# Kernel optimization log

Measured on AMD Instinct MI355X. Metric: run time of the kernel, lower is better.

The kernel has to match this reference:

```python
import jax, jax.numpy as jnp
import numpy as np

B, T, C, N = 4, 1024, 960, 64
H = C // N
R_W, R_A, R_V, R_G = 64, 64, 32, 128
LN_EPS = 0.00064


def setup_inputs() -> dict:
    key = jax.random.key(0)
    ks = jax.random.split(key, 28)
    s = 0.5 / np.sqrt(C)
    u = lambda k, sh, sc: jax.random.uniform(k, sh, jnp.float32, -sc, sc)
    n = lambda k, sh, sc: jax.random.normal(k, sh, jnp.float32) * sc
    return {
        "x": jax.random.normal(ks[0], (B, T, C), jnp.float32),
        "v_first": jax.random.normal(ks[1], (B, T, C), jnp.float32),
        "x_r": jax.random.uniform(ks[2], (1, 1, C), jnp.float32),
        "x_w": jax.random.uniform(ks[3], (1, 1, C), jnp.float32),
        "x_k": jax.random.uniform(ks[4], (1, 1, C), jnp.float32),
        "x_v": jax.random.uniform(ks[5], (1, 1, C), jnp.float32),
        "x_a": jax.random.uniform(ks[6], (1, 1, C), jnp.float32),
        "x_g": jax.random.uniform(ks[7], (1, 1, C), jnp.float32),
        "w0": n(ks[8], (1, 1, C), 0.5) - 2.0,
        "w1": n(ks[9], (C, R_W), 0.02),
        "w2": n(ks[10], (R_W, C), 0.02),
        "a0": n(ks[11], (1, 1, C), 0.3),
        "a1": n(ks[12], (C, R_A), 0.02),
        "a2": n(ks[13], (R_A, C), 0.02),
        "v0": n(ks[14], (1, 1, C), 0.3) + 0.73,
        "v1": n(ks[15], (C, R_V), 0.02),
        "v2": n(ks[16], (R_V, C), 0.02),
        "g1": n(ks[17], (C, R_G), 0.02),
        "g2": n(ks[18], (R_G, C), 0.02),
        "k_k": n(ks[19], (1, 1, C), 0.1) + 0.71,
        "k_a": n(ks[20], (1, 1, C), 0.1) + 1.02,
        "r_k": n(ks[21], (H, N), 0.1) - 0.04,
        "Wr": u(ks[22], (C, C), s),
        "Wk": u(ks[23], (C, C), 0.1 * s),
        "Wv": u(ks[24], (C, C), s),
        "Wo": u(ks[25], (C, C), s),
        "ln_g": jnp.ones((C,), jnp.float32),
        "ln_b": jnp.zeros((C,), jnp.float32),
    }


def reference(x, v_first, x_r, x_w, x_k, x_v, x_a, x_g, w0, w1, w2,
              a0, a1, a2, v0, v1, v2, g1, g2, k_k, k_a, r_k,
              Wr, Wk, Wv, Wo, ln_g, ln_b):
    Bx, Tx, Cx = x.shape
    # token shift: xx[t] = x[t-1] - x[t], with x[-1] = 0
    xx = jnp.concatenate([jnp.zeros_like(x[:, :1]), x[:, :-1]], axis=1) - x
    xr = x + xx * x_r; xw = x + xx * x_w; xk = x + xx * x_k
    xv = x + xx * x_v; xa = x + xx * x_a; xg = x + xx * x_g
    r = xr @ Wr
    w_raw = w0 + jnp.tanh(xw @ w1) @ w2       # log-space decay
    k = xk @ Wk
    v = xv @ Wv
    # layer_id > 0: residual mix with layer-0 value
    v = v + (v_first - v) * jax.nn.sigmoid(v0 + (xv @ v1) @ v2)
    a = jax.nn.sigmoid(a0 + (xa @ a1) @ a2)   # in-context learning rate
    g = jax.nn.sigmoid(xg @ g1) @ g2          # gate
    kk = (k * k_k).reshape(Bx, Tx, H, N)
    kk = kk / jnp.maximum(jnp.linalg.norm(kk, axis=-1, keepdims=True), 1e-12)
    k = k * (1.0 + (a - 1.0) * k_a)
    f32 = jnp.float32
    rh = r.reshape(Bx, Tx, H, N).astype(f32)
    kh = k.reshape(Bx, Tx, H, N).astype(f32)
    vh = v.reshape(Bx, Tx, H, N).astype(f32)
    wh = jnp.exp(-jax.nn.softplus(-w_raw.reshape(Bx, Tx, H, N).astype(f32)) - 0.5)
    ah = (-kk).astype(f32)                              # removal key
    bh = (kk * a.reshape(Bx, Tx, H, N)).astype(f32)     # replacement key

    def step(state, inp):
        r_t, w_t, k_t, v_t, a_t, b_t = inp  # each (B,H,N); state (B,H,N,N)
        sa = jnp.einsum('bhij,bhj->bhi', state, a_t)
        state = (state * w_t[:, :, None, :]
                 + sa[..., None] * b_t[:, :, None, :]
                 + v_t[..., None] * k_t[:, :, None, :])
        out_t = jnp.einsum('bhij,bhj->bhi', state, r_t)
        return state, out_t

    tm = lambda u: jnp.transpose(u, (1, 0, 2, 3))  # time-major
    state0 = jnp.zeros((Bx, H, N, N), f32)
    _, wkv = jax.lax.scan(step, state0, (tm(rh), tm(wh), tm(kh), tm(vh), tm(ah), tm(bh)))
    wkv = jnp.transpose(wkv, (1, 0, 2, 3))  # (B,T,H,N)
    # GroupNorm with H groups == per-head layernorm over N
    mu = wkv.mean(-1, keepdims=True)
    var = wkv.var(-1, keepdims=True)
    xn = (wkv - mu) / jnp.sqrt(var + LN_EPS)
    xn = xn * ln_g.reshape(H, N) + ln_b.reshape(H, N)
    bonus = (rh * kh * r_k).sum(-1, keepdims=True) * vh  # r*k*v bonus term
    xo = (xn + bonus).astype(x.dtype).reshape(Bx, Tx, Cx)
    return (xo * g) @ Wo


if __name__ == "__main__":
    out = reference(**setup_inputs())
    print(out.shape, out.dtype)
```

## Files before the change

kernel.cpp:

```cpp
#include <hip/hip_runtime.h>
#include <hip/hip_bf16.h>
#include <math.h>

#define Tn 1024
#define Cn 960
#define Hn 15
#define Nn 64
#define Mn 4096

typedef short bf16x8 __attribute__((ext_vector_type(8)));
typedef float f32x4 __attribute__((ext_vector_type(4)));

#define MCc ((size_t)Mn * Cn)

__device__ __forceinline__ float sigmf(float x) { return 1.0f / (1.0f + __expf(-x)); }

__device__ __forceinline__ ushort f2bf(float x) {
    unsigned u = __float_as_uint(x);
    unsigned r = (u + 0x7FFFu + ((u >> 16) & 1u)) >> 16;
    return (ushort)r;
}
__device__ __forceinline__ float bf2f(ushort h) { return __uint_as_float(((unsigned)h) << 16); }

__device__ __forceinline__ float rowsum16(float x) {
    x += __int_as_float(__builtin_amdgcn_update_dpp(0, __float_as_int(x), 0x121, 0xF, 0xF, true));
    x += __int_as_float(__builtin_amdgcn_update_dpp(0, __float_as_int(x), 0x122, 0xF, 0xF, true));
    x += __int_as_float(__builtin_amdgcn_update_dpp(0, __float_as_int(x), 0x124, 0xF, 0xF, true));
    x += __int_as_float(__builtin_amdgcn_update_dpp(0, __float_as_int(x), 0x128, 0xF, 0xF, true));
    return x;
}

__global__ __launch_bounds__(256) void mix6_kernel(
    const float* __restrict__ x,
    const float* __restrict__ mr, const float* __restrict__ mw, const float* __restrict__ mk,
    const float* __restrict__ mv, const float* __restrict__ ma, const float* __restrict__ mg,
    ushort* __restrict__ r_sp, ushort* __restrict__ w_sp, ushort* __restrict__ k_sp,
    ushort* __restrict__ v_sp, ushort* __restrict__ a_sp, ushort* __restrict__ g_sp)
{
    int idx = blockIdx.x * 256 + threadIdx.x;
    int e = idx * 4;
    if (e >= Mn * Cn) return;
    int m = e / Cn;
    int c = e - m * Cn;
    int t = m & (Tn - 1);
    float4 xv = *(const float4*)(x + e);
    float4 xp = make_float4(0.f, 0.f, 0.f, 0.f);
    if (t > 0) xp = *(const float4*)(x + e - Cn);
    float4 dx = make_float4(xp.x - xv.x, xp.y - xv.y, xp.z - xv.z, xp.w - xv.w);
#define MIXSPLIT(MIXP, P)                                                     \
    {                                                                         \
        float4 mm = *(const float4*)(MIXP + c);                               \
        float4 O = make_float4(xv.x + dx.x * mm.x, xv.y + dx.y * mm.y,        \
                               xv.z + dx.z * mm.z, xv.w + dx.w * mm.w);       \
        ushort h0 = f2bf(O.x), h1 = f2bf(O.y), h2 = f2bf(O.z), h3 = f2bf(O.w);\
        ushort l0 = f2bf(O.x - bf2f(h0)), l1 = f2bf(O.y - bf2f(h1));          \
        ushort l2 = f2bf(O.z - bf2f(h2)), l3 = f2bf(O.w - bf2f(h3));          \
        *(ushort4*)(P + e) = make_ushort4(h0, h1, h2, h3);                    \
        *(ushort4*)(P + MCc + e) = make_ushort4(l0, l1, l2, l3);              \
    }
    MIXSPLIT(mr, r_sp)
    MIXSPLIT(mw, w_sp)
    MIXSPLIT(mk, k_sp)
    MIXSPLIT(mv, v_sp)
    MIXSPLIT(ma, a_sp)
    MIXSPLIT(mg, g_sp)
#undef MIXSPLIT
}

__global__ __launch_bounds__(256) void convWT_kernel(
    const float* __restrict__ W, ushort* __restrict__ Thi, ushort* __restrict__ Tlo)
{
    __shared__ float tile[32][33];
    int k0 = blockIdx.x * 32, n0 = blockIdx.y * 32;
    int tx = threadIdx.x & 31, ty = threadIdx.x >> 5;
#pragma unroll
    for (int i = 0; i < 4; ++i)
        tile[ty + 8 * i][tx] = W[(size_t)(k0 + ty + 8 * i) * 960 + n0 + tx];
    __syncthreads();
#pragma unroll
    for (int i = 0; i < 4; ++i) {
        float x = tile[tx][ty + 8 * i];
        ushort h = f2bf(x);
        ushort l = f2bf(x - bf2f(h));
        size_t o = (size_t)(n0 + ty + 8 * i) * 960 + k0 + tx;
        Thi[o] = h;
        Tlo[o] = l;
    }
}

__global__ __launch_bounds__(256) void convWT3_kernel(
    const float* __restrict__ Wr, const float* __restrict__ Wk,
    const float* __restrict__ Wv,
    ushort* __restrict__ S0, ushort* __restrict__ S1, ushort* __restrict__ S2)
{
    __shared__ float tile[32][33];
    int z = blockIdx.z;
    const float* W = (z == 0) ? Wr : (z == 1) ? Wk : Wv;
    ushort* Thi = (z == 0) ? S0 : (z == 1) ? S1 : S2;
    ushort* Tlo = Thi + (size_t)960 * 960;
    int k0 = blockIdx.x * 32, n0 = blockIdx.y * 32;
    int tx = threadIdx.x & 31, ty = threadIdx.x >> 5;
#pragma unroll
    for (int i = 0; i < 4; ++i)
        tile[ty + 8 * i][tx] = W[(size_t)(k0 + ty + 8 * i) * 960 + n0 + tx];
    __syncthreads();
#pragma unroll
    for (int i = 0; i < 4; ++i) {
        float x = tile[tx][ty + 8 * i];
        ushort h = f2bf(x);
        ushort l = f2bf(x - bf2f(h));
        size_t o = (size_t)(n0 + ty + 8 * i) * 960 + k0 + tx;
        Thi[o] = h;
        Tlo[o] = l;
    }
}

__global__ __launch_bounds__(256) void wprep_kernel(
    const float* __restrict__ w1, const float* __restrict__ a1,
    const float* __restrict__ v1, const float* __restrict__ g1,
    const float* __restrict__ w2, const float* __restrict__ a2,
    const float* __restrict__ v2, const float* __restrict__ g2,
    ushort* __restrict__ arena)
{
    __shared__ float tile[32][33];
    int z = blockIdx.z;
    const float* src;
    int K, N;
    size_t off;
    switch (z) {
        case 0: src = w1; K = 960; N = 64;  off = 0;      break;
        case 1: src = a1; K = 960; N = 64;  off = 122880; break;
        case 2: src = v1; K = 960; N = 32;  off = 245760; break;
        case 3: src = g1; K = 960; N = 128; off = 307200; break;
        case 4: src = w2; K = 64;  N = 960; off = 552960; break;
        case 5: src = a2; K = 64;  N = 960; off = 675840; break;
        case 6: src = v2; K = 32;  N = 960; off = 798720; break;
        default: src = g2; K = 128; N = 960; off = 860160; break;
    }
    int k0 = blockIdx.x * 32, n0 = blockIdx.y * 32;
    if (k0 >= K || n0 >= N) return;
    int tx = threadIdx.x & 31, ty = threadIdx.x >> 5;
#pragma unroll
    for (int i = 0; i < 4; ++i)
        tile[ty + 8 * i][tx] = src[(size_t)(k0 + ty + 8 * i) * N + n0 + tx];
    __syncthreads();
    ushort* Thi = arena + off;
    ushort* Tlo = arena + off + (size_t)K * N;
#pragma unroll
    for (int i = 0; i < 4; ++i) {
        float x = tile[tx][ty + 8 * i];
        ushort h = f2bf(x);
        ushort l = f2bf(x - bf2f(h));
        size_t o = (size_t)(n0 + ty + 8 * i) * K + k0 + tx;
        Thi[o] = h;
        Tlo[o] = l;
    }
}

__global__ __launch_bounds__(256) void convN_kernel(
    const float* __restrict__ X, ushort* __restrict__ hi, ushort* __restrict__ lo, int n4)
{
    int idx = blockIdx.x * 256 + threadIdx.x;
    if (idx >= n4) return;
    int e = idx * 4;
    float4 x = *(const float4*)(X + e);
    ushort h0 = f2bf(x.x), h1 = f2bf(x.y), h2 = f2bf(x.z), h3 = f2bf(x.w);
    ushort l0 = f2bf(x.x - bf2f(h0)), l1 = f2bf(x.y - bf2f(h1));
    ushort l2 = f2bf(x.z - bf2f(h2)), l3 = f2bf(x.w - bf2f(h3));
    *(ushort4*)(hi + e) = make_ushort4(h0, h1, h2, h3);
    *(ushort4*)(lo + e) = make_ushort4(l0, l1, l2, l3);
}

__device__ __forceinline__ void gemm_core(
    const ushort* __restrict__ Ahi, const ushort* __restrict__ Alo,
    const ushort* __restrict__ Bhi, const ushort* __restrict__ Blo,
    float* __restrict__ C, int ldc, int bm, int bn)
{
    __shared__ __align__(16) ushort sA[2][2][128][40];
    __shared__ __align__(16) ushort sB[2][2][64][40];
    const int K = 960;
    int t = threadIdx.x;
    int w = t >> 6, l = t & 63;
    int lr = l & 15, lk = l >> 4;

    int ar = t >> 1, aseg = t & 1;
    int br = t & 63, bhalf = (t >> 6) & 1, bseg = t >> 7;
    const ushort* gAh = Ahi + (size_t)(bm + ar) * K + aseg * 16;
    const ushort* gAl = Alo + (size_t)(bm + ar) * K + aseg * 16;
    const ushort* gB = (bhalf ? Blo : Bhi) + (size_t)(bn + br) * K + bseg * 16;

    f32x4 acc[2][4];
#pragma unroll
    for (int i = 0; i < 2; ++i)
#pragma unroll
        for (int j = 0; j < 4; ++j)
#pragma unroll
            for (int e = 0; e < 4; ++e) acc[i][j][e] = 0.f;

    float4 h0P, h1P, l0P, l1P, b0P, b1P;
    float4 h0Q, h1Q, l0Q, l1Q, b0Q, b1Q;
#define LOADP(KOFF)                                                           \
    {                                                                         \
        h0P = *(const float4*)(gAh + (KOFF));                                 \
        h1P = *(const float4*)(gAh + (KOFF) + 8);                             \
        l0P = *(const float4*)(gAl + (KOFF));                                 \
        l1P = *(const float4*)(gAl + (KOFF) + 8);                             \
        b0P = *(const float4*)(gB + (KOFF));                                  \
        b1P = *(const float4*)(gB + (KOFF) + 8);                              \
    }
#define LOADQ(KOFF)                                                           \
    {                                                                         \
        h0Q = *(const float4*)(gAh + (KOFF));                                 \
        h1Q = *(const float4*)(gAh + (KOFF) + 8);                             \
        l0Q = *(const float4*)(gAl + (KOFF));                                 \
        l1Q = *(const float4*)(gAl + (KOFF) + 8);                             \
        b0Q = *(const float4*)(gB + (KOFF));                                  \
        b1Q = *(const float4*)(gB + (KOFF) + 8);                              \
    }
#define WRITEP(BUF)                                                           \
    {                                                                         \
        *(float4*)&sA[BUF][0][ar][aseg * 16] = h0P;                           \
        *(float4*)&sA[BUF][0][ar][aseg * 16 + 8] = h1P;                       \
        *(float4*)&sA[BUF][1][ar][aseg * 16] = l0P;                           \
        *(float4*)&sA[BUF][1][ar][aseg * 16 + 8] = l1P;                       \
        *(float4*)&sB[BUF][bhalf][br][bseg * 16] = b0P;                       \
        *(float4*)&sB[BUF][bhalf][br][bseg * 16 + 8] = b1P;                   \
    }
#define WRITEQ(BUF)                                                           \
    {                                                                         \
        *(float4*)&sA[BUF][0][ar][aseg * 16] = h0Q;                           \
        *(float4*)&sA[BUF][0][ar][aseg * 16 + 8] = h1Q;                       \
        *(float4*)&sA[BUF][1][ar][aseg * 16] = l0Q;                           \
        *(float4*)&sA[BUF][1][ar][aseg * 16 + 8] = l1Q;                       \
        *(float4*)&sB[BUF][bhalf][br][bseg * 16] = b0Q;                       \
        *(float4*)&sB[BUF][bhalf][br][bseg * 16 + 8] = b1Q;                   \
    }
#define COMPUTEK(BUF)                                                         \
    {                                                                         \
        bf16x8 ah[2], al[2], bh[4], bl[4];                                    \
        _Pragma("unroll")                                                     \
        for (int i = 0; i < 2; ++i) {                                         \
            ah[i] = *(const bf16x8*)&sA[BUF][0][32 * w + 16 * i + lr][lk * 8];\
            al[i] = *(const bf16x8*)&sA[BUF][1][32 * w + 16 * i + lr][lk * 8];\
        }                                                                     \
        _Pragma("unroll")                                                     \
        for (int j = 0; j < 4; ++j) {                                         \
            bh[j] = *(const bf16x8*)&sB[BUF][0][16 * j + lr][lk * 8];         \
            bl[j] = *(const bf16x8*)&sB[BUF][1][16 * j + lr][lk * 8];         \
        }                                                                     \
        _Pragma("unroll")                                                     \
        for (int i = 0; i < 2; ++i)                                           \
            _Pragma("unroll")                                                 \
            for (int j = 0; j < 4; ++j) {                                     \
                acc[i][j] = __builtin_amdgcn_mfma_f32_16x16x32_bf16(          \
                    ah[i], bh[j], acc[i][j], 0, 0, 0);                        \
                acc[i][j] = __builtin_amdgcn_mfma_f32_16x16x32_bf16(          \
                    ah[i], bl[j], acc[i][j], 0, 0, 0);                        \
                acc[i][j] = __builtin_amdgcn_mfma_f32_16x16x32_bf16(          \
                    al[i], bh[j], acc[i][j], 0, 0, 0);                        \
            }                                                                 \
    }

    LOADP(0)
    WRITEP(0)
    LOADQ(32)
    asm volatile("s_waitcnt lgkmcnt(0)" ::: "memory");
    __builtin_amdgcn_s_barrier();

    int cur = 0;
    for (int ks = 0; ks < 30; ks += 2) {
        int k2 = (ks + 2 < 30 ? ks + 2 : 29) * 32;
        LOADP(k2)
        COMPUTEK(cur)
        WRITEQ(cur ^ 1)
        asm volatile("s_waitcnt lgkmcnt(0)" ::: "memory");
        __builtin_amdgcn_s_barrier();
        cur ^= 1;
        int k3 = (ks + 3 < 30 ? ks + 3 : 29) * 32;
        LOADQ(k3)
        COMPUTEK(cur)
        WRITEP(cur ^ 1)
        asm volatile("s_waitcnt lgkmcnt(0)" ::: "memory");
        __builtin_amdgcn_s_barrier();
        cur ^= 1;
    }

#pragma unroll
    for (int i = 0; i < 2; ++i)
#pragma unroll
        for (int j = 0; j < 4; ++j)
#pragma unroll
            for (int jr = 0; jr < 4; ++jr) {
                int row = bm + 32 * w + 16 * i + lk * 4 + jr;
                int col = bn + 16 * j + lr;
                C[(size_t)row * ldc + col] = acc[i][j][jr];
            }
#undef COMPUTEK
#undef WRITEP
#undef WRITEQ
#undef LOADP
#undef LOADQ
}

__global__ __launch_bounds__(256) void gemm3_kernel(
    const ushort* __restrict__ XR, const ushort* __restrict__ XK,
    const ushort* __restrict__ XV,
    const ushort* __restrict__ WrS, const ushort* __restrict__ WkS,
    const ushort* __restrict__ WvS,
    float* __restrict__ oR, float* __restrict__ oK, float* __restrict__ oV)
{
    int z = blockIdx.z;
    const ushort* A = (z == 0) ? XR : (z == 1) ? XK : XV;
    const ushort* W = (z == 0) ? WrS : (z == 1) ? WkS : WvS;
    float* C = (z == 0) ? oR : (z == 1) ? oK : oV;
    gemm_core(A, A + MCc, W, W + (size_t)960 * 960, C, Cn,
              blockIdx.x * 128, blockIdx.y * 64);
}

__global__ __launch_bounds__(256) void gemm1_kernel(
    const ushort* __restrict__ Ahi, const ushort* __restrict__ Alo,
    const ushort* __restrict__ Bhi, const ushort* __restrict__ Blo,
    float* __restrict__ C, int ldc)
{
    gemm_core(Ahi, Alo, Bhi, Blo, C, ldc, blockIdx.x * 128, blockIdx.y * 64);
}

__device__ __forceinline__ void lora_core(
    const ushort* __restrict__ Ahi, const ushort* __restrict__ Alo, int lda,
    const ushort* __restrict__ Bhi, const ushort* __restrict__ Blo,
    float* __restrict__ C, int ldc, int Nvalid, int K, int act, int bn)
{
    __shared__ __align__(16) ushort sA[2][2][128][40];
    __shared__ __align__(16) ushort sB[2][2][64][40];
    int bm = blockIdx.x * 128;
    int t = threadIdx.x;
    int w = t >> 6, l = t & 63;
    int lr = l & 15, lk = l >> 4;

    int ar = t >> 2, aseg = t & 3;
    int brr = t >> 2;
    int bhl = brr >> 6, brow = brr & 63, bseg = t & 3;
    const ushort* gAh = Ahi + (size_t)(bm + ar) * lda + aseg * 8;
    const ushort* gAl = Alo + (size_t)(bm + ar) * lda + aseg * 8;
    const ushort* gB = (bhl ? Blo : Bhi) + (size_t)(bn + brow) * K + bseg * 8;

    f32x4 acc[4];
#pragma unroll
    for (int j = 0; j < 4; ++j)
#pragma unroll
        for (int e = 0; e < 4; ++e) acc[j][e] = 0.f;

    float4 rhP, rlP, rbP, rhQ, rlQ, rbQ;
#define LLOADP(KOFF)                                                          \
    {                                                                         \
        rhP = *(const float4*)(gAh + (KOFF));                                 \
        rlP = *(const float4*)(gAl + (KOFF));                                 \
        rbP = *(const float4*)(gB + (KOFF));                                  \
    }
#define LLOADQ(KOFF)                                                          \
    {                                                                         \
        rhQ = *(const float4*)(gAh + (KOFF));                                 \
        rlQ = *(const float4*)(gAl + (KOFF));                                 \
        rbQ = *(const float4*)(gB + (KOFF));                                  \
    }
#define LWRITEP(BUF)                                                          \
    {                                                                         \
        *(float4*)&sA[BUF][0][ar][aseg * 8] = rhP;                            \
        *(float4*)&sA[BUF][1][ar][aseg * 8] = rlP;                            \
        *(float4*)&sB[BUF][bhl][brow][bseg * 8] = rbP;                        \
    }
#define LWRITEQ(BUF)                                                          \
    {                                                                         \
        *(float4*)&sA[BUF][0][ar][aseg * 8] = rhQ;                            \
        *(float4*)&sA[BUF][1][ar][aseg * 8] = rlQ;                            \
        *(float4*)&sB[BUF][bhl][brow][bseg * 8] = rbQ;                        \
    }
#define LCOMPUTE(BUF)                                                         \
    {                                                                         \
        bf16x8 ah, al, bh[4], bl[4];                                          \
        ah = *(const bf16x8*)&sA[BUF][0][16 * w + lr][lk * 8];                \
        al = *(const bf16x8*)&sA[BUF][1][16 * w + lr][lk * 8];                \
        _Pragma("unroll")                                                     \
        for (int j = 0; j < 4; ++j) {                                         \
            bh[j] = *(const bf16x8*)&sB[BUF][0][16 * j + lr][lk * 8];         \
            bl[j] = *(const bf16x8*)&sB[BUF][1][16 * j + lr][lk * 8];         \
        }                                                                     \
        _Pragma("unroll")                                                     \
        for (int j = 0; j < 4; ++j) {                                         \
            acc[j] = __builtin_amdgcn_mfma_f32_16x16x32_bf16(ah, bh[j], acc[j], 0, 0, 0); \
            acc[j] = __builtin_amdgcn_mfma_f32_16x16x32_bf16(ah, bl[j], acc[j], 0, 0, 0); \
            acc[j] = __builtin_amdgcn_mfma_f32_16x16x32_bf16(al, bh[j], acc[j], 0, 0, 0); \
        }                                                                     \
    }

    int nk = K >> 5;
    LLOADP(0)
    LWRITEP(0)
    if (nk > 1) LLOADQ(32)
    asm volatile("s_waitcnt lgkmcnt(0)" ::: "memory");
    __builtin_amdgcn_s_barrier();

    int cur = 0;
    for (int ks = 0; ks < nk; ++ks) {
        int k2 = (ks + 2 < nk ? ks + 2 : nk - 1) * 32;
        if (!(ks & 1)) { LLOADP(k2) } else { LLOADQ(k2) }
        LCOMPUTE(cur)
        if (ks + 1 < nk) {
            if (!(ks & 1)) { LWRITEQ(cur ^ 1) } else { LWRITEP(cur ^ 1) }
            asm volatile("s_waitcnt lgkmcnt(0)" ::: "memory");
            __builtin_amdgcn_s_barrier();
        }
        cur ^= 1;
    }

#pragma unroll
    for (int j = 0; j < 4; ++j)
#pragma unroll
        for (int jr = 0; jr < 4; ++jr) {
            int row = bm + 16 * w + lk * 4 + jr;
            int col = bn + 16 * j + lr;
            if (col < Nvalid) {
                float v = acc[j][jr];
                if (act == 1) v = tanhf(v);
                else if (act == 2) v = sigmf(v);
                C[(size_t)row * ldc + col] = v;
            }
        }
#undef LCOMPUTE
#undef LWRITEP
#undef LWRITEQ
#undef LLOADP
#undef LLOADQ
}

__global__ __launch_bounds__(512) void lora_down_kernel(
    const ushort* __restrict__ xw_sp, const ushort* __restrict__ xa_sp,
    const ushort* __restrict__ xv_sp, const ushort* __restrict__ xg_sp,
    const ushort* __restrict__ arena, float* __restrict__ hid)
{
    int z = blockIdx.z;
    int bn = blockIdx.y * 64;
    const ushort* A;
    size_t off;
    int N, act, coff;
    switch (z) {
        case 0: A = xw_sp; off = 0;      N = 64;  act = 1; coff = 0;   break;
        case 1: A = xa_sp; off = 122880; N = 64;  act = 0; coff = 64;  break;
        case 2: A = xv_sp; off = 245760; N = 32;  act = 0; coff = 128; break;
        default: A = xg_sp; off = 307200; N = 128; act = 2; coff = 160; break;
    }
    if (bn >= N) return;
    lora_core(A, A + MCc, Cn, arena + off, arena + off + (size_t)960 * N,
              hid + coff, 288, N, 960, act, bn);
}

__global__ __launch_bounds__(512) void lora_up_kernel(
    const ushort* __restrict__ hidHi, const ushort* __restrict__ hidLo,
    const ushort* __restrict__ arena,
    float* __restrict__ oW, float* __restrict__ oA,
    float* __restrict__ oV, float* __restrict__ oG)
{
    int z = blockIdx.z;
    int bn = blockIdx.y * 64;
    size_t off;
    int K, aoff;
    float* C;
    switch (z) {
        case 0: off = 552960; K = 64;  aoff = 0;   C = oW; break;
        case 1: off = 675840; K = 64;  aoff = 64;  C = oA; break;
        case 2: off = 798720; K = 32;  aoff = 128; C = oV; break;
        default: off = 860160; K = 128; aoff = 160; C = oG; break;
    }
    lora_core(hidHi + aoff, hidLo + aoff, 288, arena + off,
              arena + off + (size_t)K * 960, C, Cn, Cn, K, 0, bn);
}

__global__ __launch_bounds__(256, 2) void scan_kernel(
    const float* __restrict__ rP, const float* __restrict__ wrawP,
    const float* __restrict__ apreP, const float* __restrict__ vsigP,
    const float* __restrict__ krawP, const float* __restrict__ vrawP,
    const float* __restrict__ vfirstP, const float* __restrict__ gP,
    const float* __restrict__ w0, const float* __restrict__ a0,
    const float* __restrict__ v0c, const float* __restrict__ kkc,
    const float* __restrict__ kac, const float* __restrict__ r_k,
    const float* __restrict__ ln_g, const float* __restrict__ ln_b,
    ushort* __restrict__ xsp)
{
    __shared__ float buf[2][7][16][64];
    __shared__ float outL[16][64];
    int tid = threadIdx.x;
    int q = tid >> 6, l = tid & 63;
    int blk = blockIdx.x;
    int bh = blk >> 3, seg = blk & 7;
    int bb = bh / Hn, h = bh - bb * Hn;
    size_t base = (size_t)bb * Tn * Cn + h * 64;
    int rg = l >> 4, cg = l & 15;
    int row0 = 16 * q + 4 * rg;
    int c0 = 4 * cg;

    int sstep = tid >> 4, sseg = tid & 15;
    size_t soff = base + (size_t)sstep * Cn + sseg * 4;
    int wofs = sstep * 64 + sseg * 4;
    int ccol = h * 64 + sseg * 4;

    int cbeg = (seg == 0) ? 0 : 8 * seg - 3;
    int cendc = 8 * seg + 8;
    int coutc = 8 * seg;

    float4 w0c4 = *(const float4*)(w0 + ccol);
    float4 a0c4 = *(const float4*)(a0 + ccol);
    float4 v0c4 = *(const float4*)(v0c + ccol);
    float4 kkc4 = *(const float4*)(kkc + ccol);
    float4 kac4 = *(const float4*)(kac + ccol);
    float4 rk4 = *(const float4*)(r_k + ccol);
    float4 lg4 = *(const float4*)(ln_g + ccol);
    float4 lb4 = *(const float4*)(ln_b + ccol);

    float s[4][4];
#pragma unroll
    for (int r = 0; r < 4; ++r)
#pragma unroll
        for (int c = 0; c < 4; ++c) s[r][c] = 0.f;

    float4 g_r, g_wr, g_vr, g_vf, g_vs, g_g, g_kr, g_ap;

#define LOADSTAGE(OFF)                                                        \
    g_r = *(const float4*)(rP + soff + (OFF));                                \
    g_wr = *(const float4*)(wrawP + soff + (OFF));                            \
    g_vr = *(const float4*)(vrawP + soff + (OFF));                            \
    g_vf = *(const float4*)(vfirstP + soff + (OFF));                          \
    g_vs = *(const float4*)(vsigP + soff + (OFF));                            \
    g_g = *(const float4*)(gP + soff + (OFF));                                \
    g_kr = *(const float4*)(krawP + soff + (OFF));                            \
    g_ap = *(const float4*)(apreP + soff + (OFF));

#define PARK(BN)                                                              \
    {                                                                         \
        const float E = 0.60653065971263342f;                                 \
        float4 w4;                                                            \
        w4.x = sigmf(w0c4.x + g_wr.x) * E;                                    \
        w4.y = sigmf(w0c4.y + g_wr.y) * E;                                    \
        w4.z = sigmf(w0c4.z + g_wr.z) * E;                                    \
        w4.w = sigmf(w0c4.w + g_wr.w) * E;                                    \
        float4 v4;                                                            \
        v4.x = g_vr.x + (g_vf.x - g_vr.x) * sigmf(v0c4.x + g_vs.x);           \
        v4.y = g_vr.y + (g_vf.y - g_vr.y) * sigmf(v0c4.y + g_vs.y);           \
        v4.z = g_vr.z + (g_vf.z - g_vr.z) * sigmf(v0c4.z + g_vs.z);           \
        v4.w = g_vr.w + (g_vf.w - g_vr.w) * sigmf(v0c4.w + g_vs.w);           \
        float4 a4;                                                            \
        a4.x = sigmf(a0c4.x + g_ap.x);                                        \
        a4.y = sigmf(a0c4.y + g_ap.y);                                        \
        a4.z = sigmf(a0c4.z + g_ap.z);                                        \
        a4.w = sigmf(a0c4.w + g_ap.w);                                        \
        float4 kk;                                                            \
        kk.x = g_kr.x * kkc4.x; kk.y = g_kr.y * kkc4.y;                       \
        kk.z = g_kr.z * kkc4.z; kk.w = g_kr.w * kkc4.w;                       \
        float ss = kk.x * kk.x + kk.y * kk.y + kk.z * kk.z + kk.w * kk.w;     \
        ss = rowsum16(ss);                                                    \
        float inv = 1.0f / fmaxf(sqrtf(ss), 1e-12f);                          \
        float4 ah4, bh4, kh4;                                                 \
        ah4.x = -kk.x * inv; bh4.x = kk.x * inv * a4.x;                       \
        ah4.y = -kk.y * inv; bh4.y = kk.y * inv * a4.y;                       \
        ah4.z = -kk.z * inv; bh4.z = kk.z * inv * a4.z;                       \
        ah4.w = -kk.w * inv; bh4.w = kk.w * inv * a4.w;                       \
        kh4.x = g_kr.x * (1.0f + (a4.x - 1.0f) * kac4.x);                     \
        kh4.y = g_kr.y * (1.0f + (a4.y - 1.0f) * kac4.y);                     \
        kh4.z = g_kr.z * (1.0f + (a4.z - 1.0f) * kac4.z);                     \
        kh4.w = g_kr.w * (1.0f + (a4.w - 1.0f) * kac4.w);                     \
        *(float4*)((BN) + 0 * 1024 + wofs) = g_r;                             \
        *(float4*)((BN) + 1 * 1024 + wofs) = w4;                              \
        *(float4*)((BN) + 2 * 1024 + wofs) = kh4;                             \
        *(float4*)((BN) + 3 * 1024 + wofs) = ah4;                             \
        *(float4*)((BN) + 4 * 1024 + wofs) = bh4;                             \
        *(float4*)((BN) + 5 * 1024 + wofs) = v4;                              \
        *(float4*)((BN) + 6 * 1024 + wofs) = g_g;                             \
    }

    LOADSTAGE((size_t)cbeg * 16 * Cn)
    PARK(&buf[0][0][0][0])
    asm volatile("s_waitcnt lgkmcnt(0)" ::: "memory");
    __builtin_amdgcn_s_barrier();

#define DECL2(S)                                                              \
    float4 S##a0, S##w0, S##k0, S##b0, S##r0, S##v0;                          \
    float4 S##a1, S##w1, S##k1, S##b1, S##r1, S##v1;
#define DSLOAD2(S, T)                                                         \
    S##a0 = *(const float4*)(bc + 3 * 1024 + (T) * 64 + c0);                  \
    S##w0 = *(const float4*)(bc + 1 * 1024 + (T) * 64 + c0);                  \
    S##k0 = *(const float4*)(bc + 2 * 1024 + (T) * 64 + c0);                  \
    S##b0 = *(const float4*)(bc + 4 * 1024 + (T) * 64 + c0);                  \
    S##r0 = *(const float4*)(bc + 0 * 1024 + (T) * 64 + c0);                  \
    S##v0 = *(const float4*)(bc + 5 * 1024 + (T) * 64 + row0);                \
    S##a1 = *(const float4*)(bc + 3 * 1024 + ((T) + 1) * 64 + c0);            \
    S##w1 = *(const float4*)(bc + 1 * 1024 + ((T) + 1) * 64 + c0);            \
    S##k1 = *(const float4*)(bc + 2 * 1024 + ((T) + 1) * 64 + c0);            \
    S##b1 = *(const float4*)(bc + 4 * 1024 + ((T) + 1) * 64 + c0);            \
    S##r1 = *(const float4*)(bc + 0 * 1024 + ((T) + 1) * 64 + c0);            \
    S##v1 = *(const float4*)(bc + 5 * 1024 + ((T) + 1) * 64 + row0);
#define STEP(AV, WV, KV, BV, RV, VV, T)                                       \
    {                                                                         \
        float sp0 = s[0][0] * AV.x + s[0][1] * AV.y + s[0][2] * AV.z + s[0][3] * AV.w; \
        float sp1 = s[1][0] * AV.x + s[1][1] * AV.y + s[1][2] * AV.z + s[1][3] * AV.w; \
        float sp2 = s[2][0] * AV.x + s[2][1] * AV.y + s[2][2] * AV.z + s[2][3] * AV.w; \
        float sp3 = s[3][0] * AV.x + s[3][1] * AV.y + s[3][2] * AV.z + s[3][3] * AV.w; \
        sp0 = rowsum16(sp0);                                                  \
        sp1 = rowsum16(sp1);                                                  \
        sp2 = rowsum16(sp2);                                                  \
        sp3 = rowsum16(sp3);                                                  \
        float sa[4] = {sp0, sp1, sp2, sp3};                                   \
        float vr[4] = {VV.x, VV.y, VV.z, VV.w};                               \
        float op[4];                                                          \
        _Pragma("unroll")                                                     \
        for (int r = 0; r < 4; ++r) {                                         \
            s[r][0] = s[r][0] * WV.x + sa[r] * BV.x + vr[r] * KV.x;           \
            float o = s[r][0] * RV.x;                                         \
            s[r][1] = s[r][1] * WV.y + sa[r] * BV.y + vr[r] * KV.y;           \
            o += s[r][1] * RV.y;                                              \
            s[r][2] = s[r][2] * WV.z + sa[r] * BV.z + vr[r] * KV.z;           \
            o += s[r][2] * RV.z;                                              \
            s[r][3] = s[r][3] * WV.w + sa[r] * BV.w + vr[r] * KV.w;           \
            o += s[r][3] * RV.w;                                              \
            op[r] = rowsum16(o);                                              \
        }                                                                     \
        if (cg == 0)                                                          \
            *(float4*)&outL[T][row0] = make_float4(op[0], op[1], op[2], op[3]); \
    }

    DECL2(A) DECL2(B)

    int cur = 0;
    for (int c = cbeg; c < cendc; ++c) {
        const float* bc = &buf[cur][0][0][0];
        {
            int cnxt = (c + 1 < cendc) ? c + 1 : c;
            LOADSTAGE((size_t)cnxt * 16 * Cn)
        }

        DSLOAD2(A, 0)
#pragma unroll
        for (int it = 0; it < 4; ++it) {
            DSLOAD2(B, 4 * it + 2)
            STEP(Aa0, Aw0, Ak0, Ab0, Ar0, Av0, 4 * it + 0)
            STEP(Aa1, Aw1, Ak1, Ab1, Ar1, Av1, 4 * it + 1)
            if (it < 3) { DSLOAD2(A, 4 * it + 4) }
            STEP(Ba0, Bw0, Bk0, Bb0, Br0, Bv0, 4 * it + 2)
            STEP(Ba1, Bw1, Bk1, Bb1, Br1, Bv1, 4 * it + 3)
        }

        PARK(&buf[cur ^ 1][0][0][0])
        asm volatile("s_waitcnt lgkmcnt(0)" ::: "memory");
        __builtin_amdgcn_s_barrier();

        if (c >= coutc) {
            float4 o4 = *(const float4*)&outL[sstep][4 * sseg];
            float4 r4 = *(const float4*)(bc + 0 * 1024 + sstep * 64 + 4 * sseg);
            float4 k4 = *(const float4*)(bc + 2 * 1024 + sstep * 64 + 4 * sseg);
            float4 v4 = *(const float4*)(bc + 5 * 1024 + sstep * 64 + 4 * sseg);
            float4 gg4 = *(const float4*)(bc + 6 * 1024 + sstep * 64 + 4 * sseg);
            float m1 = o4.x + o4.y + o4.z + o4.w;
            float m2 = o4.x * o4.x + o4.y * o4.y + o4.z * o4.z + o4.w * o4.w;
            float bd = r4.x * k4.x * rk4.x + r4.y * k4.y * rk4.y +
                       r4.z * k4.z * rk4.z + r4.w * k4.w * rk4.w;
            m1 = rowsum16(m1);
            m2 = rowsum16(m2);
            bd = rowsum16(bd);
            float mean = m1 * (1.f / 64.f);
            float var = m2 * (1.f / 64.f) - mean * mean;
            float is = rsqrtf(var + 0.00064f);
            float xo0 = ((o4.x - mean) * is * lg4.x + lb4.x + bd * v4.x) * gg4.x;
            float xo1 = ((o4.y - mean) * is * lg4.y + lb4.y + bd * v4.y) * gg4.y;
            float xo2 = ((o4.z - mean) * is * lg4.z + lb4.z + bd * v4.z) * gg4.z;
            float xo3 = ((o4.w - mean) * is * lg4.w + lb4.w + bd * v4.w) * gg4.w;
            ushort h0 = f2bf(xo0), h1 = f2bf(xo1), h2 = f2bf(xo2), h3 = f2bf(xo3);
            ushort l0 = f2bf(xo0 - bf2f(h0)), l1 = f2bf(xo1 - bf2f(h1));
            ushort l2 = f2bf(xo2 - bf2f(h2)), l3 = f2bf(xo3 - bf2f(h3));
            size_t gt = (size_t)c * 16 + sstep;
            size_t eo = base + gt * Cn + 4 * sseg;
            *(ushort4*)(xsp + eo) = make_ushort4(h0, h1, h2, h3);
            *(ushort4*)(xsp + MCc + eo) = make_ushort4(l0, l1, l2, l3);
        }
        __builtin_amdgcn_s_barrier();
        cur ^= 1;
    }
#undef STEP
#undef DSLOAD2
#undef DECL2
#undef PARK
#undef LOADSTAGE
}

extern "C" void kernel_launch(void* const* d_in, const int* in_sizes, int n_in,
                              void* d_out, int out_size, void* d_ws, size_t ws_size,
                              hipStream_t stream)
{
    const float* x       = (const float*)d_in[0];
    const float* v_first = (const float*)d_in[1];
    const float* x_r     = (const float*)d_in[2];
    const float* x_w     = (const float*)d_in[3];
    const float* x_k     = (const float*)d_in[4];
    const float* x_v     = (const float*)d_in[5];
    const float* x_a     = (const float*)d_in[6];
    const float* x_g     = (const float*)d_in[7];
    const float* w0      = (const float*)d_in[8];
    const float* w1      = (const float*)d_in[9];
    const float* w2      = (const float*)d_in[10];
    const float* a0      = (const float*)d_in[11];
    const float* a1      = (const float*)d_in[12];
    const float* a2      = (const float*)d_in[13];
    const float* v0c     = (const float*)d_in[14];
    const float* v1      = (const float*)d_in[15];
    const float* v2      = (const float*)d_in[16];
    const float* g1w     = (const float*)d_in[17];
    const float* g2w     = (const float*)d_in[18];
    const float* k_k     = (const float*)d_in[19];
    const float* k_a     = (const float*)d_in[20];
    const float* r_k     = (const float*)d_in[21];
    const float* Wr      = (const float*)d_in[22];
    const float* Wk      = (const float*)d_in[23];
    const float* Wv      = (const float*)d_in[24];
    const float* Wo      = (const float*)d_in[25];
    const float* ln_g    = (const float*)d_in[26];
    const float* ln_b    = (const float*)d_in[27];
    float* out = (float*)d_out;

    float* ws = (float*)d_ws;
    float* B0 = ws + 0 * MCc;
    float* B1 = ws + 1 * MCc;
    float* B2 = ws + 2 * MCc;
    float* B3 = ws + 3 * MCc;
    float* B4 = ws + 4 * MCc;
    float* B5 = ws + 5 * MCc;
    float* B6 = ws + 6 * MCc;
    float* B7 = ws + 7 * MCc;
    float* B8 = ws + 8 * MCc;
    float* hid = ws + 9 * MCc;

    ushort* XRsp = (ushort*)B0;
    ushort* XWsp = (ushort*)B1;
    ushort* XKsp = (ushort*)B2;
    ushort* XVsp = (ushort*)out;
    ushort* XAsp = (ushort*)B4;
    ushort* XGsp = (ushort*)B5;
    ushort* S3 = (ushort*)B3;
    ushort* hidHi = S3;
    ushort* hidLo = S3 + 1179648;
    ushort* arena = S3 + 2359296;
    ushort* WkS = S3 + 3465216;
    ushort* WvS = S3 + 5308416;
    ushort* WrS = (ushort*)hid;
    ushort* Whi = (ushort*)hid;
    ushort* Wlo = Whi + (size_t)960 * 960;
    ushort* Xsp = (ushort*)B4;

    mix6_kernel<<<3840, 256, 0, stream>>>(x, x_r, x_w, x_k, x_v, x_a, x_g,
                                          XRsp, XWsp, XKsp, XVsp, XAsp, XGsp);
    wprep_kernel<<<dim3(30, 30, 8), 256, 0, stream>>>(w1, a1, v1, g1w,
                                                      w2, a2, v2, g2w, arena);
    convWT3_kernel<<<dim3(30, 30, 3), 256, 0, stream>>>(Wr, Wk, Wv,
                                                        WrS, WkS, WvS);
    gemm3_kernel<<<dim3(32, 15, 3), 256, 0, stream>>>(XRsp, XKsp, XVsp,
                                                      WrS, WkS, WvS,
                                                      B6, B7, B8);
    lora_down_kernel<<<dim3(32, 2, 4), 512, 0, stream>>>(XWsp, XAsp, XVsp, XGsp,
                                                         arena, hid);
    convN_kernel<<<1152, 256, 0, stream>>>(hid, hidHi, hidLo, Mn * 288 / 4);
    lora_up_kernel<<<dim3(32, 15, 4), 512, 0, stream>>>(hidHi, hidLo, arena,
                                                        B0, B2, B1, B5);
    convWT_kernel<<<dim3(30, 30), 256, 0, stream>>>(Wo, Whi, Wlo);
    scan_kernel<<<480, 256, 0, stream>>>(B6, B0, B2, B1, B7, B8, v_first, B5,
                                         w0, a0, v0c, k_k, k_a,
                                         r_k, ln_g, ln_b, Xsp);
    gemm1_kernel<<<dim3(32, 15), 256, 0, stream>>>(Xsp, Xsp + MCc, Whi, Wlo,
                                                   out, Cn);
}
```

Baseline: 332.7 us.

## Stage GEMM tiles via direct global-to-LDS loads instead of register staging

Replaces register-staged global loads plus LDS writes in the split-bf16 GEMM core with global_load_lds direct transfers, and removes the LDS row padding to fit that instruction's contiguous layout. Each wave loads its own A rows and B rows per k-step with a simpler single-buffer-ahead pipeline. This cuts VGPR pressure and LDS store instructions, but the unpadded 64-byte rows may cause LDS bank conflicts on the bf16x8 fragment reads, and the prefetch distance shrinks from two stages to one.

```diff
diff --git a/kernel.cpp b/kernel.cpp
--- a/kernel.cpp
+++ b/kernel.cpp
@@ -29,6 +29,11 @@
     x += __int_as_float(__builtin_amdgcn_update_dpp(0, __float_as_int(x), 0x128, 0xF, 0xF, true));
     return x;
 }
+
+#define GLOAD16(GPTR, LPTR)                                                   \
+    __builtin_amdgcn_global_load_lds(                                         \
+        (const __attribute__((address_space(1))) unsigned*)(GPTR),            \
+        (__attribute__((address_space(3))) unsigned*)(LPTR), 16, 0, 0)
 
 __global__ __launch_bounds__(256) void mix6_kernel(
     const float* __restrict__ x,
@@ -176,18 +181,21 @@
     const ushort* __restrict__ Bhi, const ushort* __restrict__ Blo,
     float* __restrict__ C, int ldc, int bm, int bn)
 {
-    __shared__ __align__(16) ushort sA[2][2][128][40];
-    __shared__ __align__(16) ushort sB[2][2][64][40];
+    __shared__ __align__(16) ushort sA[2][2][128][32];
+    __shared__ __align__(16) ushort sB[2][2][64][32];
     const int K = 960;
     int t = threadIdx.x;
     int w = t >> 6, l = t & 63;
     int lr = l & 15, lk = l >> 4;
 
-    int ar = t >> 1, aseg = t & 1;
-    int br = t & 63, bhalf = (t >> 6) & 1, bseg = t >> 7;
-    const ushort* gAh = Ahi + (size_t)(bm + ar) * K + aseg * 16;
-    const ushort* gAl = Alo + (size_t)(bm + ar) * K + aseg * 16;
-    const ushort* gB = (bhalf ? Blo : Bhi) + (size_t)(bn + br) * K + bseg * 16;
+    int srow = l >> 2;
+    int skc = (l & 3) * 8;
+    const ushort* gA0h = Ahi + (size_t)(bm + 32 * w + srow) * K + skc;
+    const ushort* gA1h = Ahi + (size_t)(bm + 32 * w + 16 + srow) * K + skc;
+    const ushort* gA0l = Alo + (size_t)(bm + 32 * w + srow) * K + skc;
+    const ushort* gA1l = Alo + (size_t)(bm + 32 * w + 16 + srow) * K + skc;
+    const ushort* gBh = Bhi + (size_t)(bn + 16 * w + srow) * K + skc;
+    const ushort* gBl = Blo + (size_t)(bn + 16 * w + srow) * K + skc;
 
     f32x4 acc[2][4];
 #pragma unroll
@@ -197,43 +205,14 @@
 #pragma unroll
             for (int e = 0; e < 4; ++e) acc[i][j][e] = 0.f;
 
-    float4 h0P, h1P, l0P, l1P, b0P, b1P;
-    float4 h0Q, h1Q, l0Q, l1Q, b0Q, b1Q;
-#define LOADP(KOFF)                                                           \
-    {                                                                         \
-        h0P = *(const float4*)(gAh + (KOFF));                                 \
-        h1P = *(const float4*)(gAh + (KOFF) + 8);                             \
-        l0P = *(const float4*)(gAl + (KOFF));                                 \
-        l1P = *(const float4*)(gAl + (KOFF) + 8);                             \
-        b0P = *(const float4*)(gB + (KOFF));                                  \
-        b1P = *(const float4*)(gB + (KOFF) + 8);                              \
-    }
-#define LOADQ(KOFF)                                                           \
-    {                                                                         \
-        h0Q = *(const float4*)(gAh + (KOFF));                                 \
-        h1Q = *(const float4*)(gAh + (KOFF) + 8);                             \
-        l0Q = *(const float4*)(gAl + (KOFF));                                 \
-        l1Q = *(const float4*)(gAl + (KOFF) + 8);                             \
-        b0Q = *(const float4*)(gB + (KOFF));                                  \
-        b1Q = *(const float4*)(gB + (KOFF) + 8);                              \
-    }
-#define WRITEP(BUF)                                                           \
-    {                                                                         \
-        *(float4*)&sA[BUF][0][ar][aseg * 16] = h0P;                           \
-        *(float4*)&sA[BUF][0][ar][aseg * 16 + 8] = h1P;                       \
-        *(float4*)&sA[BUF][1][ar][aseg * 16] = l0P;                           \
-        *(float4*)&sA[BUF][1][ar][aseg * 16 + 8] = l1P;                       \
-        *(float4*)&sB[BUF][bhalf][br][bseg * 16] = b0P;                       \
-        *(float4*)&sB[BUF][bhalf][br][bseg * 16 + 8] = b1P;                   \
-    }
-#define WRITEQ(BUF)                                                           \
-    {                                                                         \
-        *(float4*)&sA[BUF][0][ar][aseg * 16] = h0Q;                           \
-        *(float4*)&sA[BUF][0][ar][aseg * 16 + 8] = h1Q;                       \
-        *(float4*)&sA[BUF][1][ar][aseg * 16] = l0Q;                           \
-        *(float4*)&sA[BUF][1][ar][aseg * 16 + 8] = l1Q;                       \
-        *(float4*)&sB[BUF][bhalf][br][bseg * 16] = b0Q;                       \
-        *(float4*)&sB[BUF][bhalf][br][bseg * 16 + 8] = b1Q;                   \
+#define STAGE(BUF, KOFF)                                                      \
+    {                                                                         \
+        GLOAD16(gA0h + (KOFF), &sA[BUF][0][32 * w][0]);                       \
+        GLOAD16(gA1h + (KOFF), &sA[BUF][0][32 * w + 16][0]);                  \
+        GLOAD16(gA0l + (KOFF), &sA[BUF][1][32 * w][0]);                       \
+        GLOAD16(gA1l + (KOFF), &sA[BUF][1][32 * w + 16][0]);                  \
+        GLOAD16(gBh + (KOFF), &sB[BUF][0][16 * w][0]);                        \
+        GLOAD16(gBl + (KOFF), &sB[BUF][1][16 * w][0]);                        \
     }
 #define COMPUTEK(BUF)                                                         \
     {                                                                         \
@@ -261,26 +240,15 @@
             }                                                                 \
     }
 
-    LOADP(0)
-    WRITEP(0)
-    LOADQ(32)
-    asm volatile("s_waitcnt lgkmcnt(0)" ::: "memory");
+    STAGE(0, 0)
+    asm volatile("s_waitcnt vmcnt(0)" ::: "memory");
     __builtin_amdgcn_s_barrier();
 
     int cur = 0;
-    for (int ks = 0; ks < 30; ks += 2) {
-        int k2 = (ks + 2 < 30 ? ks + 2 : 29) * 32;
-        LOADP(k2)
+    for (int ks = 0; ks < 30; ++ks) {
+        if (ks + 1 < 30) STAGE(cur ^ 1, (ks + 1) * 32)
         COMPUTEK(cur)
-        WRITEQ(cur ^ 1)
-        asm volatile("s_waitcnt lgkmcnt(0)" ::: "memory");
-        __builtin_amdgcn_s_barrier();
-        cur ^= 1;
-        int k3 = (ks + 3 < 30 ? ks + 3 : 29) * 32;
-        LOADQ(k3)
-        COMPUTEK(cur)
-        WRITEP(cur ^ 1)
-        asm volatile("s_waitcnt lgkmcnt(0)" ::: "memory");
+        asm volatile("s_waitcnt vmcnt(0) lgkmcnt(0)" ::: "memory");
         __builtin_amdgcn_s_barrier();
         cur ^= 1;
     }
@@ -296,10 +264,7 @@
                 C[(size_t)row * ldc + col] = acc[i][j][jr];
             }
 #undef COMPUTEK
-#undef WRITEP
-#undef WRITEQ
-#undef LOADP
-#undef LOADQ
+#undef STAGE
 }
 
 __global__ __launch_bounds__(256) void gemm3_kernel(
```

Result: faster. 314.1 us (-5.6%).
